# Kernel optimization log

Measured on AMD Instinct MI355X. Metric: run time of the kernel, lower is better.

Reference implementation:

```python
import jax, jax.numpy as jnp
import numpy as np

BLOCK = 64  # block_size from config
NEG_INF = -1e9


def setup_inputs() -> dict:
    key = jax.random.key(0)
    k1, k2, k3, k4 = jax.random.split(key, 4)
    B, H, S, D = 2, 8, 2048, 64
    nb = S // BLOCK  # 32 blocks per side
    query = jax.random.normal(k1, (B, H, S, D), dtype=jnp.float32)
    key_t = jax.random.normal(k2, (B, H, S, D), dtype=jnp.float32)
    value = jax.random.normal(k3, (B, H, S, D), dtype=jnp.float32)
    # binary block mask; force diagonal blocks on so every row has >=1 valid key
    mat = jax.random.randint(k4, (nb, nb), 0, 2).astype(jnp.int32)
    mat = mat.at[jnp.arange(nb), jnp.arange(nb)].set(1)
    mask = jnp.ones((B, S), dtype=jnp.float32)  # padding mask (1 = keep)
    return {"query": query, "key": key_t, "value": value, "mask": mask, "mat": mat}


def reference(query, key, value, mask, mat):
    # Upsample block mask [nb, nb] -> dense [S, S] (nearest, like nn.Upsample)
    block_dense = jnp.repeat(jnp.repeat(mat, BLOCK, axis=0), BLOCK, axis=1) > 0
    # Block-sparse QK^T: only positions inside nonzero blocks participate.
    scores = jnp.einsum('bhqd,bhkd->bhqk', query, key)
    # Additive padding-mask bias, as in the original: 1e6 * (1 - mask)
    scores = scores - 1e6 * (1.0 - mask)[:, None, None, :]
    # Positions outside the block pattern are excluded from the softmax.
    scores = jnp.where(block_dense[None, None, :, :], scores, NEG_INF)
    attn = jax.nn.softmax(scores, axis=-1)
    out = jnp.einsum('bhqk,bhkd->bhqd', attn, value)
    return out
```

## Files before the change

### kernel.cpp

```cpp
#include <hip/hip_runtime.h>


typedef __attribute__((ext_vector_type(8))) short short8;
typedef __attribute__((ext_vector_type(4))) short short4_;
typedef __attribute__((ext_vector_type(4))) float float4_;
typedef __attribute__((ext_vector_type(8))) _Float16 half8_;

#define B_   2
#define H_   8
#define S_   2048
#define D_   64
#define NB_  32
#define KP   72
#define LOG2E 1.4426950408889634f

__device__ __forceinline__ short f2bf(float f) {
    union { float f; unsigned int u; } x; x.f = f;
    unsigned int r = x.u + 0x7FFFu + ((x.u >> 16) & 1u);
    return (short)(r >> 16);
}
__device__ __forceinline__ short f2bf_t(float f) {
    union { float f; unsigned int u; } x; x.f = f;
    return (short)(x.u >> 16);
}
__device__ __forceinline__ float bf2f(short s) {
    union { unsigned int u; float f; } x; x.u = ((unsigned int)(unsigned short)s) << 16;
    return x.f;
}
__device__ __forceinline__ short f2h(float f) {
    _Float16 h = (_Float16)f;
    return __builtin_bit_cast(short, h);
}
__device__ __forceinline__ int swz(int row, int gran) {
    return (row << 6) + (((gran ^ row) & 7) << 3);
}

__global__ __launch_bounds__(256)
void preconvert_kernel(const float* __restrict__ K, const float* __restrict__ V,
                       short* __restrict__ Khf, short* __restrict__ Vtb) {
    __shared__ short vn[64 * KP];
    const int tid = threadIdx.x;
    const int kt  = blockIdx.x;
    const int bh  = blockIdx.y;
    const size_t tb = ((size_t)bh * S_ + kt * 64) * D_;

#pragma unroll
    for (int it = 0; it < 4; ++it) {
        int i = tid + it * 256;
        int row = i >> 4, c4 = (i & 15) * 4;
        float4_ kv = *(const float4_*)(K + tb + row * D_ + c4);
        short4_ kh;
#pragma unroll
        for (int e = 0; e < 4; ++e) kh[e] = f2h(kv[e] * LOG2E);
        *(short4_*)(Khf + tb + row * D_ + c4) = kh;
        float4_ vv = *(const float4_*)(V + tb + row * D_ + c4);
        short4_ vb;
#pragma unroll
        for (int e = 0; e < 4; ++e) vb[e] = f2bf(vv[e]);
        *(short4_*)&vn[row * KP + c4] = vb;
    }
    __syncthreads();
#pragma unroll
    for (int it = 0; it < 2; ++it) {
        int i = tid + it * 256;
        int rowd = i >> 3, key8 = (i & 7) * 8;
        short8 o;
#pragma unroll
        for (int e = 0; e < 8; ++e) o[e] = vn[(key8 + e) * KP + rowd];
        *(short8*)(Vtb + (((size_t)(bh * NB_ + kt)) * 64 + rowd) * 64 + key8) = o;
    }
}

__global__ __launch_bounds__(512, 4)
void attn_fused(const float* __restrict__ Q,
                const float* __restrict__ Msk,
                const int* __restrict__ Mat,
                float* __restrict__ O,
                const short* __restrict__ Khf_g,
                const short* __restrict__ Vtb_g) {
    __shared__ __align__(16) short lds[16384 + 8 * 16 * KP];

    const int tid  = threadIdx.x;
    const int wave = tid >> 6;
    const int half = wave >> 2;
    const int qtw  = wave & 3;
    const int lane = tid & 63;
    const int c    = lane & 15;
    const int quad = lane >> 4;
    const int hid  = tid & 255;

    const int qb = blockIdx.x;
    const int bh = blockIdx.y;
    const int b  = bh / H_;
    const size_t base = (size_t)bh * S_ * D_;

    const int hbK = half * 4096;
    const int hbV = 8192 + half * 4096;

    half8_ qa0, qa1;
    {
        const float* qp = Q + base + (size_t)(qb * 64 + qtw * 16 + c) * D_ + quad * 8;
#pragma unroll
        for (int e = 0; e < 8; ++e) {
            qa0[e] = (_Float16)qp[e];
            qa1[e] = (_Float16)qp[e + 32];
        }
    }

    float4_ o[4];
    float l_part[4];
#pragma unroll
    for (int t = 0; t < 4; ++t) { o[t][0] = 0.f; o[t][1] = 0.f; o[t][2] = 0.f; o[t][3] = 0.f; }
#pragma unroll
    for (int j = 0; j < 4; ++j) l_part[j] = 0.f;

    unsigned long long bmv = __ballot(Mat[qb * NB_ + (lane & 31)] != 0);
    unsigned int mb = (unsigned int)(bmv & 0xFFFFFFFFull);
    const int nact  = __popc(mb);
    const int niter = (nact + 1) >> 1;
    unsigned int mine = 0;
    {
        unsigned int tb2 = mb; int idx = 0;
        while (tb2) {
            int k = __builtin_ctz(tb2); tb2 &= tb2 - 1;
            if ((idx & 1) == half) mine |= (1u << k);
            ++idx;
        }
    }

    int srow[2], sgrn[2], soff[2];
#pragma unroll
    for (int it = 0; it < 2; ++it) {
        int i = hid + it * 256;
        srow[it] = i >> 3;
        sgrn[it] = i & 7;
        soff[it] = swz(srow[it], sgrn[it]);
    }
    int foff_lo[4], foff_hi[4];
#pragma unroll
    for (int t = 0; t < 4; ++t) {
        foff_lo[t] = swz(t * 16 + c, quad);
        foff_hi[t] = swz(t * 16 + c, quad + 4);
    }

    short8 sK[2], sV[2];
    float  biasn[4];
    int kb; bool kill;
    if (mine) { kb = __builtin_ctz(mine); mine &= mine - 1; kill = false; }
    else      { kb = __builtin_ctz(mb); kill = true; }
    {
        const short* kh = Khf_g + base + (size_t)kb * 64 * D_;
        const short* vt = Vtb_g + ((size_t)(bh * NB_ + kb)) * 64 * 64;
#pragma unroll
        for (int it = 0; it < 2; ++it) {
            sK[it] = *(const short8*)(kh + srow[it] * 64 + sgrn[it] * 8);
            sV[it] = *(const short8*)(vt + srow[it] * 64 + sgrn[it] * 8);
        }
#pragma unroll
        for (int t = 0; t < 4; ++t)
            biasn[t] = kill ? -2.0e6f
                            : -1.0e6f * LOG2E * (1.0f - Msk[(size_t)b * S_ + kb * 64 + t * 16 + c]);
    }

    for (int it2 = 0; it2 < niter; ++it2) {
        __syncthreads();
#pragma unroll
        for (int s = 0; s < 2; ++s) {
            *(short8*)&lds[hbK + soff[s]] = sK[s];
            *(short8*)&lds[hbV + soff[s]] = sV[s];
        }
        float biasc[4];
#pragma unroll
        for (int t = 0; t < 4; ++t) biasc[t] = biasn[t];
        __syncthreads();

        if (it2 + 1 < niter) {
            if (mine) { kb = __builtin_ctz(mine); mine &= mine - 1; kill = false; }
            else      { kill = true; }
            if (!kill) {
                const short* kh = Khf_g + base + (size_t)kb * 64 * D_;
                const short* vt = Vtb_g + ((size_t)(bh * NB_ + kb)) * 64 * 64;
#pragma unroll
                for (int s = 0; s < 2; ++s) {
                    sK[s] = *(const short8*)(kh + srow[s] * 64 + sgrn[s] * 8);
                    sV[s] = *(const short8*)(vt + srow[s] * 64 + sgrn[s] * 8);
                }
#pragma unroll
                for (int t = 0; t < 4; ++t)
                    biasn[t] = -1.0e6f * LOG2E * (1.0f - Msk[(size_t)b * S_ + kb * 64 + t * 16 + c]);
            } else {
#pragma unroll
                for (int t = 0; t < 4; ++t) biasn[t] = -2.0e6f;
            }
        }

        float4_ sc[4];
#pragma unroll
        for (int t = 0; t < 4; ++t) { sc[t][0] = 0.f; sc[t][1] = 0.f; sc[t][2] = 0.f; sc[t][3] = 0.f; }
#pragma unroll
        for (int t = 0; t < 4; ++t) {
            half8_ kb0 = __builtin_bit_cast(half8_, *(const short8*)&lds[hbK + foff_lo[t]]);
            half8_ kb1 = __builtin_bit_cast(half8_, *(const short8*)&lds[hbK + foff_hi[t]]);
            sc[t] = __builtin_amdgcn_mfma_f32_16x16x32_f16(qa0, kb0, sc[t], 0, 0, 0);
            sc[t] = __builtin_amdgcn_mfma_f32_16x16x32_f16(qa1, kb1, sc[t], 0, 0, 0);
        }

        const int pwoff = 16384 + wave * 16 * KP;
#pragma unroll
        for (int t = 0; t < 4; ++t) {
#pragma unroll
            for (int j = 0; j < 4; ++j) {
                float p = exp2f(sc[t][j] + biasc[t]);
                l_part[j] += p;
                lds[pwoff + (quad * 4 + j) * KP + t * 16 + c] = f2bf_t(p);
            }
        }

        const short* pp = &lds[pwoff + c * KP + quad * 8];
        short8 pa0 = *(const short8*)(pp);
        short8 pa1 = *(const short8*)(pp + 32);

#pragma unroll
        for (int t = 0; t < 4; ++t) {
            short8 vb0 = *(const short8*)&lds[hbV + foff_lo[t]];
            short8 vb1 = *(const short8*)&lds[hbV + foff_hi[t]];
            o[t] = __builtin_amdgcn_mfma_f32_16x16x32_bf16(pa0, vb0, o[t], 0, 0, 0);
            o[t] = __builtin_amdgcn_mfma_f32_16x16x32_bf16(pa1, vb1, o[t], 0, 0, 0);
        }
    }

    __syncthreads();
    float* fl = (float*)lds;
    if (half == 1) {
        const int idx = ((wave - 4) * 64 + lane) * 21;
#pragma unroll
        for (int t = 0; t < 4; ++t)
#pragma unroll
            for (int j = 0; j < 4; ++j) fl[idx + t * 4 + j] = o[t][j];
#pragma unroll
        for (int j = 0; j < 4; ++j) fl[idx + 16 + j] = l_part[j];
    }
    __syncthreads();
    if (half == 0) {
        const int idx = (wave * 64 + lane) * 21;
#pragma unroll
        for (int j = 0; j < 4; ++j) {
            float rs = l_part[j] + fl[idx + 16 + j];
            rs += __shfl_xor(rs, 1);
            rs += __shfl_xor(rs, 2);
            rs += __shfl_xor(rs, 4);
            rs += __shfl_xor(rs, 8);
            float inv = 1.0f / rs;
            size_t rowoff = base + (size_t)(qb * 64 + qtw * 16 + quad * 4 + j) * D_;
#pragma unroll
            for (int t = 0; t < 4; ++t)
                O[rowoff + t * 16 + c] = (o[t][j] + fl[idx + t * 4 + j]) * inv;
        }
    }
}

__global__ __launch_bounds__(256, 2)
void attn_mfma_fb(const float* __restrict__ Q,
                  const float* __restrict__ K,
                  const float* __restrict__ V,
                  const float* __restrict__ Msk,
                  const int* __restrict__ Mat,
                  float* __restrict__ O) {
    __shared__ __align__(16) short lds[4 * 64 * KP];
    short* Khi = lds;
    short* Klo = lds + 64 * KP;
    short* Vt  = lds + 2 * 64 * KP;
    short* Pl  = lds + 3 * 64 * KP;

    const int tid  = threadIdx.x;
    const int wave = tid >> 6;
    const int lane = tid & 63;
    const int c    = lane & 15;
    const int quad = lane >> 4;

    const int qb = blockIdx.x;
    const int bh = blockIdx.y;
    const int b  = bh / H_;
    const size_t base = (size_t)bh * S_ * D_;

    short8 qh0, qh1, ql0, ql1;
    {
        const float* qp = Q + base + (size_t)(qb * 64 + wave * 16 + c) * D_ + quad * 8;
#pragma unroll
        for (int e = 0; e < 8; ++e) {
            float f0 = qp[e], f1 = qp[e + 32];
            qh0[e] = f2bf(f0); ql0[e] = f2bf(f0 - bf2f(qh0[e]));
            qh1[e] = f2bf(f1); ql1[e] = f2bf(f1 - bf2f(qh1[e]));
        }
    }

    float4_ o[4];
    float l_part[4];
#pragma unroll
    for (int t = 0; t < 4; ++t) { o[t][0] = 0.f; o[t][1] = 0.f; o[t][2] = 0.f; o[t][3] = 0.f; }
#pragma unroll
    for (int j = 0; j < 4; ++j) l_part[j] = 0.f;

    for (int kb = 0; kb < NB_; ++kb) {
        if (Mat[qb * NB_ + kb] == 0) continue;

        __syncthreads();
        {
            const float* kg = K + base + (size_t)kb * 64 * D_;
            const float* vg = V + base + (size_t)kb * 64 * D_;
#pragma unroll
            for (int it = 0; it < 4; ++it) {
                int i = tid + it * 256;
                int row = i >> 4, c4 = (i & 15) * 4;
                float4_ kv = *(const float4_*)(kg + row * D_ + c4);
                short4_ hi, lo;
#pragma unroll
                for (int e = 0; e < 4; ++e) {
                    hi[e] = f2bf(kv[e]);
                    lo[e] = f2bf(kv[e] - bf2f(hi[e]));
                }
                *(short4_*)&Khi[row * KP + c4] = hi;
                *(short4_*)&Klo[row * KP + c4] = lo;
                float4_ vv = *(const float4_*)(vg + row * D_ + c4);
#pragma unroll
                for (int e = 0; e < 4; ++e) Vt[(c4 + e) * KP + row] = f2bf(vv[e]);
            }
        }
        __syncthreads();

        float4_ sc[4];
#pragma unroll
        for (int t = 0; t < 4; ++t) { sc[t][0] = 0.f; sc[t][1] = 0.f; sc[t][2] = 0.f; sc[t][3] = 0.f; }
#pragma unroll
        for (int t = 0; t < 4; ++t) {
            const short* kph = &Khi[(t * 16 + c) * KP + quad * 8];
            const short* kpl = &Klo[(t * 16 + c) * KP + quad * 8];
            short8 kh0 = *(const short8*)(kph);
            short8 kh1 = *(const short8*)(kph + 32);
            short8 kl0 = *(const short8*)(kpl);
            short8 kl1 = *(const short8*)(kpl + 32);
            sc[t] = __builtin_amdgcn_mfma_f32_16x16x32_bf16(qh0, kh0, sc[t], 0, 0, 0);
            sc[t] = __builtin_amdgcn_mfma_f32_16x16x32_bf16(qh1, kh1, sc[t], 0, 0, 0);
            sc[t] = __builtin_amdgcn_mfma_f32_16x16x32_bf16(qh0, kl0, sc[t], 0, 0, 0);
            sc[t] = __builtin_amdgcn_mfma_f32_16x16x32_bf16(qh1, kl1, sc[t], 0, 0, 0);
            sc[t] = __builtin_amdgcn_mfma_f32_16x16x32_bf16(ql0, kh0, sc[t], 0, 0, 0);
            sc[t] = __builtin_amdgcn_mfma_f32_16x16x32_bf16(ql1, kh1, sc[t], 0, 0, 0);
        }

        short* Pw = Pl + wave * 16 * KP;
#pragma unroll
        for (int t = 0; t < 4; ++t) {
            float bias = -1.0e6f * (1.0f - Msk[(size_t)b * S_ + kb * 64 + t * 16 + c]);
#pragma unroll
            for (int j = 0; j < 4; ++j) {
                float p = __expf(sc[t][j] + bias);
                l_part[j] += p;
                Pw[(quad * 4 + j) * KP + t * 16 + c] = f2bf(p);
            }
        }

        const short* pp = Pl + wave * 16 * KP + c * KP + quad * 8;
        short8 pa0 = *(const short8*)(pp);
        short8 pa1 = *(const short8*)(pp + 32);

#pragma unroll
        for (int t = 0; t < 4; ++t) {
            const short* vp = &Vt[(t * 16 + c) * KP + quad * 8];
            short8 vb0 = *(const short8*)(vp);
            short8 vb1 = *(const short8*)(vp + 32);
            o[t] = __builtin_amdgcn_mfma_f32_16x16x32_bf16(pa0, vb0, o[t], 0, 0, 0);
            o[t] = __builtin_amdgcn_mfma_f32_16x16x32_bf16(pa1, vb1, o[t], 0, 0, 0);
        }
    }

#pragma unroll
    for (int j = 0; j < 4; ++j) {
        float rs = l_part[j];
        rs += __shfl_xor(rs, 1);
        rs += __shfl_xor(rs, 2);
        rs += __shfl_xor(rs, 4);
        rs += __shfl_xor(rs, 8);
        float inv = 1.0f / rs;
        size_t rowoff = base + (size_t)(qb * 64 + wave * 16 + quad * 4 + j) * D_;
#pragma unroll
        for (int t = 0; t < 4; ++t)
            O[rowoff + t * 16 + c] = o[t][j] * inv;
    }
}

extern "C" void kernel_launch(void* const* d_in, const int* in_sizes, int n_in,
                              void* d_out, int out_size, void* d_ws, size_t ws_size,
                              hipStream_t stream) {
    const float* q   = (const float*)d_in[0];
    const float* k   = (const float*)d_in[1];
    const float* v   = (const float*)d_in[2];
    const float* msk = (const float*)d_in[3];
    const int*   mat = (const int*)d_in[4];
    float*       out = (float*)d_out;

    const size_t elems = (size_t)B_ * H_ * S_ * D_;
    const size_t need  = 2 * elems * sizeof(short);
    const int use_pre  = (ws_size >= need) ? 1 : 0;

    short* khf = (short*)d_ws;
    short* vtb = khf + elems;

    if (use_pre) {
        dim3 pgrid(NB_, B_ * H_);
        preconvert_kernel<<<pgrid, dim3(256), 0, stream>>>(k, v, khf, vtb);
        dim3 grid(NB_, B_ * H_);
        attn_fused<<<grid, dim3(512), 0, stream>>>(q, msk, mat, out, khf, vtb);
    } else {
        dim3 grid(NB_, B_ * H_);
        attn_mfma_fb<<<grid, dim3(256), 0, stream>>>(q, k, v, msk, mat, out);
    }
}
```

Measured before the change: 108.7 us.

## Double-buffer K/V tiles via direct global-to-LDS loads with pre-swizzled layouts

```diff
diff --git a/kernel.cpp b/kernel.cpp
--- a/kernel.cpp
+++ b/kernel.cpp
@@ -34,40 +34,48 @@
 __device__ __forceinline__ int swz(int row, int gran) {
     return (row << 6) + (((gran ^ row) & 7) << 3);
 }
+__device__ __forceinline__ void gload16(const short* g, short* l) {
+    __builtin_amdgcn_global_load_lds(
+        (const __attribute__((address_space(1))) void*)g,
+        (__attribute__((address_space(3))) void*)l, 16, 0, 0);
+}
 
 __global__ __launch_bounds__(256)
 void preconvert_kernel(const float* __restrict__ K, const float* __restrict__ V,
                        short* __restrict__ Khf, short* __restrict__ Vtb) {
-    __shared__ short vn[64 * KP];
     const int tid = threadIdx.x;
     const int kt  = blockIdx.x;
     const int bh  = blockIdx.y;
-    const size_t tb = ((size_t)bh * S_ + kt * 64) * D_;
+    const size_t src = ((size_t)bh * S_ + kt * 64) * D_;
+    const size_t dst = ((size_t)(bh * NB_ + kt)) << 12;
 
 #pragma unroll
     for (int it = 0; it < 4; ++it) {
         int i = tid + it * 256;
         int row = i >> 4, c4 = (i & 15) * 4;
-        float4_ kv = *(const float4_*)(K + tb + row * D_ + c4);
+        float4_ kv = *(const float4_*)(K + src + row * D_ + c4);
         short4_ kh;
 #pragma unroll
         for (int e = 0; e < 4; ++e) kh[e] = f2h(kv[e] * LOG2E);
-        *(short4_*)(Khf + tb + row * D_ + c4) = kh;
-        float4_ vv = *(const float4_*)(V + tb + row * D_ + c4);
-        short4_ vb;
-#pragma unroll
-        for (int e = 0; e < 4; ++e) vb[e] = f2bf(vv[e]);
-        *(short4_*)&vn[row * KP + c4] = vb;
-    }
-    __syncthreads();
-#pragma unroll
-    for (int it = 0; it < 2; ++it) {
-        int i = tid + it * 256;
-        int rowd = i >> 3, key8 = (i & 7) * 8;
-        short8 o;
-#pragma unroll
-        for (int e = 0; e < 8; ++e) o[e] = vn[(key8 + e) * KP + rowd];
-        *(short8*)(Vtb + (((size_t)(bh * NB_ + kt)) * 64 + rowd) * 64 + key8) = o;
+        *(short4_*)(Khf + dst + swz(row, c4 >> 3) + (c4 & 7)) = kh;
+    }
+
+    {
+        const int key4 = (tid >> 4) << 2;
+        const int d4   = (tid & 15) << 2;
+        const float* vp = V + src + (size_t)key4 * D_ + d4;
+        float4_ r0 = *(const float4_*)(vp);
+        float4_ r1 = *(const float4_*)(vp + D_);
+        float4_ r2 = *(const float4_*)(vp + 2 * D_);
+        float4_ r3 = *(const float4_*)(vp + 3 * D_);
+#pragma unroll
+        for (int cc = 0; cc < 4; ++cc) {
+            short4_ col;
+            col[0] = f2bf(r0[cc]); col[1] = f2bf(r1[cc]);
+            col[2] = f2bf(r2[cc]); col[3] = f2bf(r3[cc]);
+            int d = d4 + cc;
+            *(short4_*)(Vtb + dst + swz(d, key4 >> 3) + (key4 & 7)) = col;
+        }
     }
 }
 
@@ -78,41 +86,20 @@
                 float* __restrict__ O,
                 const short* __restrict__ Khf_g,
                 const short* __restrict__ Vtb_g) {
-    __shared__ __align__(16) short lds[16384 + 8 * 16 * KP];
+    __shared__ __align__(16) short lds[40960];
 
     const int tid  = threadIdx.x;
     const int wave = tid >> 6;
     const int half = wave >> 2;
-    const int qtw  = wave & 3;
+    const int w4   = wave & 3;
     const int lane = tid & 63;
     const int c    = lane & 15;
     const int quad = lane >> 4;
-    const int hid  = tid & 255;
 
     const int qb = blockIdx.x;
     const int bh = blockIdx.y;
     const int b  = bh / H_;
     const size_t base = (size_t)bh * S_ * D_;
-
-    const int hbK = half * 4096;
-    const int hbV = 8192 + half * 4096;
-
-    half8_ qa0, qa1;
-    {
-        const float* qp = Q + base + (size_t)(qb * 64 + qtw * 16 + c) * D_ + quad * 8;
-#pragma unroll
-        for (int e = 0; e < 8; ++e) {
-            qa0[e] = (_Float16)qp[e];
-            qa1[e] = (_Float16)qp[e + 32];
-        }
-    }
-
-    float4_ o[4];
-    float l_part[4];
-#pragma unroll
-    for (int t = 0; t < 4; ++t) { o[t][0] = 0.f; o[t][1] = 0.f; o[t][2] = 0.f; o[t][3] = 0.f; }
-#pragma unroll
-    for (int j = 0; j < 4; ++j) l_part[j] = 0.f;
 
     unsigned long long bmv = __ballot(Mat[qb * NB_ + (lane & 31)] != 0);
     unsigned int mb = (unsigned int)(bmv & 0xFFFFFFFFull);
@@ -128,105 +115,125 @@
         }
     }
 
-    int srow[2], sgrn[2], soff[2];
-#pragma unroll
-    for (int it = 0; it < 2; ++it) {
-        int i = hid + it * 256;
-        srow[it] = i >> 3;
-        sgrn[it] = i & 7;
-        soff[it] = swz(srow[it], sgrn[it]);
-    }
-    int foff_lo[4], foff_hi[4];
-#pragma unroll
-    for (int t = 0; t < 4; ++t) {
-        foff_lo[t] = swz(t * 16 + c, quad);
-        foff_hi[t] = swz(t * 16 + c, quad + 4);
-    }
-
-    short8 sK[2], sV[2];
-    float  biasn[4];
     int kb; bool kill;
     if (mine) { kb = __builtin_ctz(mine); mine &= mine - 1; kill = false; }
     else      { kb = __builtin_ctz(mb); kill = true; }
     {
-        const short* kh = Khf_g + base + (size_t)kb * 64 * D_;
-        const short* vt = Vtb_g + ((size_t)(bh * NB_ + kb)) * 64 * 64;
-#pragma unroll
-        for (int it = 0; it < 2; ++it) {
-            sK[it] = *(const short8*)(kh + srow[it] * 64 + sgrn[it] * 8);
-            sV[it] = *(const short8*)(vt + srow[it] * 64 + sgrn[it] * 8);
-        }
-#pragma unroll
-        for (int t = 0; t < 4; ++t)
-            biasn[t] = kill ? -2.0e6f
-                            : -1.0e6f * LOG2E * (1.0f - Msk[(size_t)b * S_ + kb * 64 + t * 16 + c]);
-    }
-
+        const size_t tb = ((size_t)(bh * NB_ + kb)) << 12;
+        const int kd = (half << 12) + (w4 << 10);
+        const short* gk = Khf_g + tb + (w4 << 10) + lane * 8;
+        const short* gv = Vtb_g + tb + (w4 << 10) + lane * 8;
+        gload16(gk,       &lds[kd]);
+        gload16(gk + 512, &lds[kd + 512]);
+        gload16(gv,       &lds[16384 + kd]);
+        gload16(gv + 512, &lds[16384 + kd + 512]);
+    }
+
+    float biasc[4], biasn[4] = {0.f, 0.f, 0.f, 0.f};
+#pragma unroll
+    for (int t = 0; t < 4; ++t)
+        biasc[t] = kill ? -2.0e6f
+                        : -1.0e6f * LOG2E * (1.0f - Msk[(size_t)b * S_ + kb * 64 + t * 16 + c]);
+
+    half8_ qa0, qa1;
+    {
+        const float* qp = Q + base + (size_t)(qb * 64 + w4 * 16 + c) * D_ + quad * 8;
+        float4_ q0 = *(const float4_*)(qp);
+        float4_ q1 = *(const float4_*)(qp + 4);
+        float4_ q2 = *(const float4_*)(qp + 32);
+        float4_ q3 = *(const float4_*)(qp + 36);
+#pragma unroll
+        for (int e = 0; e < 4; ++e) {
+            qa0[e]     = (_Float16)q0[e];
+            qa0[e + 4] = (_Float16)q1[e];
+            qa1[e]     = (_Float16)q2[e];
+            qa1[e + 4] = (_Float16)q3[e];
+        }
+    }
+
+    float4_ o[4];
+    float l_part[4];
+#pragma unroll
+    for (int t = 0; t < 4; ++t) { o[t][0] = 0.f; o[t][1] = 0.f; o[t][2] = 0.f; o[t][3] = 0.f; }
+#pragma unroll
+    for (int j = 0; j < 4; ++j) l_part[j] = 0.f;
+
+    int foff_lo[4], foff_hi[4];
+#pragma unroll
+    for (int t = 0; t < 4; ++t) {
+        foff_lo[t] = swz(t * 16 + c, quad);
+        foff_hi[t] = swz(t * 16 + c, quad + 4);
+    }
+    const int pwoff = 32768 + (wave << 10);
+    const int prd0  = pwoff + swz(c, quad);
+    const int prd1  = pwoff + swz(c, quad + 4);
+
+    int cur = 0;
     for (int it2 = 0; it2 < niter; ++it2) {
+        bool nkill = true;
+        if (it2 + 1 < niter && mine) { kb = __builtin_ctz(mine); mine &= mine - 1; nkill = false; }
+
         __syncthreads();
-#pragma unroll
-        for (int s = 0; s < 2; ++s) {
-            *(short8*)&lds[hbK + soff[s]] = sK[s];
-            *(short8*)&lds[hbV + soff[s]] = sV[s];
-        }
-        float biasc[4];
-#pragma unroll
-        for (int t = 0; t < 4; ++t) biasc[t] = biasn[t];
-        __syncthreads();
 
         if (it2 + 1 < niter) {
-            if (mine) { kb = __builtin_ctz(mine); mine &= mine - 1; kill = false; }
-            else      { kill = true; }
-            if (!kill) {
-                const short* kh = Khf_g + base + (size_t)kb * 64 * D_;
-                const short* vt = Vtb_g + ((size_t)(bh * NB_ + kb)) * 64 * 64;
-#pragma unroll
-                for (int s = 0; s < 2; ++s) {
-                    sK[s] = *(const short8*)(kh + srow[s] * 64 + sgrn[s] * 8);
-                    sV[s] = *(const short8*)(vt + srow[s] * 64 + sgrn[s] * 8);
-                }
-#pragma unroll
-                for (int t = 0; t < 4; ++t)
-                    biasn[t] = -1.0e6f * LOG2E * (1.0f - Msk[(size_t)b * S_ + kb * 64 + t * 16 + c]);
-            } else {
-#pragma unroll
-                for (int t = 0; t < 4; ++t) biasn[t] = -2.0e6f;
+            const size_t tb = ((size_t)(bh * NB_ + kb)) << 12;
+            const int kd = ((cur ^ 1) << 13) + (half << 12) + (w4 << 10);
+            const short* gk = Khf_g + tb + (w4 << 10) + lane * 8;
+            const short* gv = Vtb_g + tb + (w4 << 10) + lane * 8;
+            gload16(gk,       &lds[kd]);
+            gload16(gk + 512, &lds[kd + 512]);
+            gload16(gv,       &lds[16384 + kd]);
+            gload16(gv + 512, &lds[16384 + kd + 512]);
+#pragma unroll
+            for (int t = 0; t < 4; ++t)
+                biasn[t] = nkill ? -2.0e6f
+                                 : -1.0e6f * LOG2E * (1.0f - Msk[(size_t)b * S_ + kb * 64 + t * 16 + c]);
+        }
+
+        const int kbase = (cur << 13) + (half << 12);
+        const int vbase = 16384 + kbase;
+
+        float4_ sc[4];
+#pragma unroll
+        for (int t = 0; t < 4; ++t) { sc[t][0] = 0.f; sc[t][1] = 0.f; sc[t][2] = 0.f; sc[t][3] = 0.f; }
+        __builtin_amdgcn_s_setprio(1);
+#pragma unroll
+        for (int t = 0; t < 4; ++t) {
+            half8_ kf0 = __builtin_bit_cast(half8_, *(const short8*)&lds[kbase + foff_lo[t]]);
+            half8_ kf1 = __builtin_bit_cast(half8_, *(const short8*)&lds[kbase + foff_hi[t]]);
+            sc[t] = __builtin_amdgcn_mfma_f32_16x16x32_f16(qa0, kf0, sc[t], 0, 0, 0);
+            sc[t] = __builtin_amdgcn_mfma_f32_16x16x32_f16(qa1, kf1, sc[t], 0, 0, 0);
+        }
+        __builtin_amdgcn_s_setprio(0);
+
+#pragma unroll
+        for (int t = 0; t < 4; ++t) {
+            const int cg = (t << 1) + (c >> 3);
+#pragma unroll
+            for (int j = 0; j < 4; ++j) {
+                float p = __builtin_amdgcn_exp2f(sc[t][j] + biasc[t]);
+                l_part[j] += p;
+                const int row = quad * 4 + j;
+                lds[pwoff + (row << 6) + (((cg ^ row) & 7) << 3) + (c & 7)] = f2bf_t(p);
             }
         }
 
-        float4_ sc[4];
-#pragma unroll
-        for (int t = 0; t < 4; ++t) { sc[t][0] = 0.f; sc[t][1] = 0.f; sc[t][2] = 0.f; sc[t][3] = 0.f; }
-#pragma unroll
-        for (int t = 0; t < 4; ++t) {
-            half8_ kb0 = __builtin_bit_cast(half8_, *(const short8*)&lds[hbK + foff_lo[t]]);
-            half8_ kb1 = __builtin_bit_cast(half8_, *(const short8*)&lds[hbK + foff_hi[t]]);
-            sc[t] = __builtin_amdgcn_mfma_f32_16x16x32_f16(qa0, kb0, sc[t], 0, 0, 0);
-            sc[t] = __builtin_amdgcn_mfma_f32_16x16x32_f16(qa1, kb1, sc[t], 0, 0, 0);
-        }
-
-        const int pwoff = 16384 + wave * 16 * KP;
-#pragma unroll
-        for (int t = 0; t < 4; ++t) {
-#pragma unroll
-            for (int j = 0; j < 4; ++j) {
-                float p = exp2f(sc[t][j] + biasc[t]);
-                l_part[j] += p;
-                lds[pwoff + (quad * 4 + j) * KP + t * 16 + c] = f2bf_t(p);
-            }
-        }
-
-        const short* pp = &lds[pwoff + c * KP + quad * 8];
-        short8 pa0 = *(const short8*)(pp);
-        short8 pa1 = *(const short8*)(pp + 32);
-
-#pragma unroll
-        for (int t = 0; t < 4; ++t) {
-            short8 vb0 = *(const short8*)&lds[hbV + foff_lo[t]];
-            short8 vb1 = *(const short8*)&lds[hbV + foff_hi[t]];
+        short8 pa0 = *(const short8*)&lds[prd0];
+        short8 pa1 = *(const short8*)&lds[prd1];
+
+        __builtin_amdgcn_s_setprio(1);
+#pragma unroll
+        for (int t = 0; t < 4; ++t) {
+            short8 vb0 = *(const short8*)&lds[vbase + foff_lo[t]];
+            short8 vb1 = *(const short8*)&lds[vbase + foff_hi[t]];
             o[t] = __builtin_amdgcn_mfma_f32_16x16x32_bf16(pa0, vb0, o[t], 0, 0, 0);
             o[t] = __builtin_amdgcn_mfma_f32_16x16x32_bf16(pa1, vb1, o[t], 0, 0, 0);
         }
+        __builtin_amdgcn_s_setprio(0);
+
+#pragma unroll
+        for (int t = 0; t < 4; ++t) biasc[t] = biasn[t];
+        cur ^= 1;
     }
 
     __syncthreads();
@@ -251,7 +258,7 @@
             rs += __shfl_xor(rs, 4);
             rs += __shfl_xor(rs, 8);
             float inv = 1.0f / rs;
-            size_t rowoff = base + (size_t)(qb * 64 + qtw * 16 + quad * 4 + j) * D_;
+            size_t rowoff = base + (size_t)(qb * 64 + w4 * 16 + quad * 4 + j) * D_;
 #pragma unroll
             for (int t = 0; t < 4; ++t)
                 O[rowoff + t * 16 + c] = (o[t][j] + fl[idx + t * 4 + j]) * inv;
```

Result: faster. 105.2 us (-3.2%).
